# Kernel optimization log

Measured on AMD Instinct MI355X. Metric: run time of the kernel, lower is better.

The kernel has to match this reference:

```python
import jax, jax.numpy as jnp
import numpy as np

B, S, H = 1, 2048, 2048
NH, KVH, D = 32, 8, 64
G = NH // KVH  # num_key_value_groups = 4


def setup_inputs() -> dict:
    key = jax.random.key(0)
    k1, k2, k3 = jax.random.split(key, 3)
    x = jax.random.normal(k1, (B, S, H), dtype=jnp.float32)
    w_qkv = jax.random.normal(k2, ((NH + 2 * KVH) * D, H), dtype=jnp.float32) * 0.02
    w_o = jax.random.normal(k3, (H, NH * D), dtype=jnp.float32) * 0.02
    return {"x": x, "w_qkv": w_qkv, "w_o": w_o}


def _rope_cos_sin(seqlen, dim, dtype):
    inv_freq = 1.0 / (10000.0 ** (jnp.arange(0, dim, 2, dtype=jnp.float32) / dim))
    t = jnp.arange(seqlen, dtype=jnp.float32)
    freqs = jnp.outer(t, inv_freq)  # [S, D/2]
    return jnp.cos(freqs).astype(dtype), jnp.sin(freqs).astype(dtype)


def _apply_rope(x, cos, sin):
    # x: [B,S,h,D]; non-interleaved half rotation (flash-attn RotaryEmbedding)
    d2 = x.shape[-1] // 2
    x1, x2 = x[..., :d2], x[..., d2:]
    c = cos[None, :, None, :]
    s = sin[None, :, None, :]
    return jnp.concatenate([x1 * c - x2 * s, x2 * c + x1 * s], axis=-1)


def reference(x, w_qkv, w_o):
    b, s, _ = x.shape
    qkv = x @ w_qkv.T  # fused QKV proj: [B,S,(NH+2*KVH)*D]
    q, kv = jnp.split(qkv, [NH * D], axis=-1)
    q = q.reshape(b, s, NH, D)
    kv = kv.reshape(b, s, 2, KVH, D)
    cos, sin = _rope_cos_sin(s, D, x.dtype)
    q = _apply_rope(q, cos, sin)
    k = _apply_rope(kv[:, :, 0], cos, sin)
    v = kv[:, :, 1]
    # GQA: group q heads per kv head instead of repeat_interleave (same math)
    qg = q.reshape(b, s, KVH, G, D)
    scale = 1.0 / np.sqrt(D).astype(np.float32)
    scores = jnp.einsum('bskgd,btkd->bkgst', qg, k) * scale  # [B,KVH,G,S,S]
    causal = jnp.tril(jnp.ones((s, s), dtype=bool))
    scores = jnp.where(causal[None, None, None], scores, jnp.asarray(-jnp.inf, scores.dtype))
    p = jax.nn.softmax(scores, axis=-1)
    out = jnp.einsum('bkgst,btkd->bskgd', p, v).reshape(b, s, NH * D)
    return out @ w_o.T
```

## Files before the change

kernel.cpp:

```cpp
#include <hip/hip_runtime.h>


typedef __bf16 bf16_t;
typedef __attribute__((ext_vector_type(8))) __bf16 bf16x8;
typedef __attribute__((ext_vector_type(4))) __bf16 bf16x4;
typedef __attribute__((ext_vector_type(4))) float f32x4;

#define S_LEN 2048
#define H_DIM 2048
#define NHEAD 32
#define KVH 8
#define HD 64
#define QKV_N 3072

#define ENT_STRIDE 8320

__global__ void cast3_kernel(const float* __restrict__ x, const float* __restrict__ wq,
                             const float* __restrict__ wo, bf16_t* __restrict__ xb,
                             bf16_t* __restrict__ wqb, bf16_t* __restrict__ wob) {
  int i = blockIdx.x * blockDim.x + threadIdx.x;
  const int n1 = S_LEN * H_DIM / 4, n2 = QKV_N * H_DIM / 4, n3 = H_DIM * H_DIM / 4;
  const float* src; bf16_t* dst; int j;
  if (i < n1)           { src = x;  dst = xb;  j = i; }
  else if (i < n1 + n2) { src = wq; dst = wqb; j = i - n1; }
  else if (i < n1 + n2 + n3) { src = wo; dst = wob; j = i - n1 - n2; }
  else return;
  float4 v = ((const float4*)src)[j];
  bf16x4 o;
  o.x = (bf16_t)v.x; o.y = (bf16_t)v.y; o.z = (bf16_t)v.z; o.w = (bf16_t)v.w;
  ((bf16x4*)dst)[j] = o;
}

__device__ __forceinline__ void async_copy16(bf16_t* lds_base, const bf16_t* g) {
  __builtin_amdgcn_global_load_lds(
      (const __attribute__((address_space(1))) unsigned int*)g,
      (__attribute__((address_space(3))) unsigned int*)lds_base, 16, 0, 0);
}

#define GBM 128
#define GBN 128

template <int EPI>
__global__ __launch_bounds__(512, 4) void gemm_sk(const bf16_t* __restrict__ A,
                                                  const bf16_t* __restrict__ B,
                                                  float* __restrict__ C,
                                                  bf16_t* __restrict__ qb,
                                                  bf16_t* __restrict__ ktp,
                                                  bf16_t* __restrict__ vt2,
                                                  int M, int N, int K) {
  __shared__ __align__(16) bf16_t As[2][GBM * 64];
  __shared__ __align__(16) bf16_t Bs[2][GBM * 64];

  const int tid  = threadIdx.x;
  const int lane = tid & 63;
  const int w    = tid >> 6;
  const int wq   = w & 3;
  const int gw   = w >> 2;
  const int wm   = (wq >> 1) * 64;
  const int wn   = (wq & 1) * 64;
  const int c    = lane & 15;
  const int quad = lane >> 4;
  const int m0   = blockIdx.y * GBM;
  const int n0   = blockIdx.x * GBN;

  f32x4 acc[4][4] = {};

  const bf16_t* Ab = A + (size_t)m0 * K;
  const bf16_t* Bb = B + (size_t)n0 * K;

  int srow[2], skc[2], sb[2];
#pragma unroll
  for (int i = 0; i < 2; ++i) {
    int p = i * 512 + tid;
    srow[i] = p >> 3;
    skc[i]  = (p & 7) ^ (srow[i] & 7);
    sb[i]   = (i * 512 + w * 64) * 8;
  }

  auto stage = [&](int buf, int k0) {
#pragma unroll
    for (int i = 0; i < 2; ++i) {
      async_copy16(&As[buf][sb[i]], Ab + (size_t)srow[i] * K + k0 + skc[i] * 8);
      async_copy16(&Bs[buf][sb[i]], Bb + (size_t)srow[i] * K + k0 + skc[i] * 8);
    }
  };

  auto compute = [&](int buf) {
    bf16x8 af[4], bfr[4];
#pragma unroll
    for (int mt = 0; mt < 4; ++mt) {
      int row = wm + mt * 16 + c;
      af[mt] = *(const bf16x8*)&As[buf][(row * 8 + ((gw * 4 + quad) ^ (row & 7))) * 8];
    }
#pragma unroll
    for (int nt = 0; nt < 4; ++nt) {
      int rowb = wn + nt * 16 + c;
      bfr[nt] = *(const bf16x8*)&Bs[buf][(rowb * 8 + ((gw * 4 + quad) ^ (rowb & 7))) * 8];
    }
#pragma unroll
    for (int mt = 0; mt < 4; ++mt)
#pragma unroll
      for (int nt = 0; nt < 4; ++nt)
        acc[mt][nt] = __builtin_amdgcn_mfma_f32_16x16x32_bf16(af[mt], bfr[nt], acc[mt][nt], 0, 0, 0);
  };

  const int NI = K >> 6;
  stage(0, 0);
  int buf = 0;
  for (int it = 0; it < NI; ++it) {
    asm volatile("s_waitcnt vmcnt(0)" ::: "memory");
    __builtin_amdgcn_s_barrier();
    if (it + 1 < NI) stage(buf ^ 1, (it + 1) << 6);
    compute(buf);
    buf ^= 1;
  }

  __syncthreads();
  float* xch = (float*)&As[0][0];
  if (gw == 1) {
#pragma unroll
    for (int t16 = 0; t16 < 16; ++t16)
      *(f32x4*)&xch[wq * 4096 + (t16 * 64 + lane) * 4] = acc[t16 >> 2][t16 & 3];
  }
  __syncthreads();
  if (gw == 0) {
#pragma unroll
    for (int t16 = 0; t16 < 16; ++t16) {
      f32x4 o = *(const f32x4*)&xch[wq * 4096 + (t16 * 64 + lane) * 4];
      acc[t16 >> 2][t16 & 3] += o;
    }

    if (EPI == 0) {
#pragma unroll
      for (int mt = 0; mt < 4; ++mt)
#pragma unroll
        for (int nt = 0; nt < 4; ++nt)
#pragma unroll
          for (int reg = 0; reg < 4; ++reg) {
            int row = m0 + wm + mt * 16 + quad * 4 + reg;
            int col = n0 + wn + nt * 16 + c;
            C[(size_t)row * N + col] = acc[mt][nt][reg];
          }
    } else {
      const int colb = n0 + wn;
      if (colb < NHEAD * HD) {
        const int h = colb >> 6;
#pragma unroll
        for (int nt = 0; nt < 2; ++nt) {
          const int i = nt * 16 + c;
          const float invf = __expf(-(float)i * (9.210340371976184f / 32.0f));
#pragma unroll
          for (int mt = 0; mt < 4; ++mt)
#pragma unroll
            for (int reg = 0; reg < 4; ++reg) {
              const int s = m0 + wm + mt * 16 + quad * 4 + reg;
              float sn, cs;
              __sincosf((float)s * invf, &sn, &cs);
              const float x1 = acc[mt][nt][reg], x2 = acc[mt][nt + 2][reg];
              bf16_t* q = qb + (size_t)s * H_DIM + h * HD;
              q[i]      = (bf16_t)((x1 * cs - x2 * sn) * 0.125f);
              q[i + 32] = (bf16_t)((x2 * cs + x1 * sn) * 0.125f);
            }
        }
      } else if (colb < NHEAD * HD + KVH * HD) {
        const int kh = (colb - NHEAD * HD) >> 6;
#pragma unroll
        for (int nt = 0; nt < 2; ++nt) {
          const int i = nt * 16 + c;
          const float invf = __expf(-(float)i * (9.210340371976184f / 32.0f));
#pragma unroll
          for (int mt = 0; mt < 4; ++mt)
#pragma unroll
            for (int reg = 0; reg < 4; ++reg) {
              const int s = m0 + wm + mt * 16 + quad * 4 + reg;
              float sn, cs;
              __sincosf((float)s * invf, &sn, &cs);
              const float x1 = acc[mt][nt][reg], x2 = acc[mt][nt + 2][reg];
              bf16_t* kd = ktp + ((size_t)kh * S_LEN + s) * HD;
              kd[i]      = (bf16_t)(x1 * cs - x2 * sn);
              kd[i + 32] = (bf16_t)(x2 * cs + x1 * sn);
            }
        }
      } else {
        const int kh = (colb - NHEAD * HD - KVH * HD) >> 6;
#pragma unroll
        for (int nt = 0; nt < 4; ++nt) {
          const int d = nt * 16 + c;
#pragma unroll
          for (int mt = 0; mt < 4; ++mt) {
            const int sr = m0 + wm + mt * 16 + quad * 4;
            bf16x4 pv;
#pragma unroll
            for (int reg = 0; reg < 4; ++reg) pv[reg] = (bf16_t)acc[mt][nt][reg];
            *(bf16x4*)&vt2[((size_t)kh * HD + d) * S_LEN + sr] = pv;
          }
        }
      }
    }
  }
}

#define PSTR 72

__global__ __launch_bounds__(256) void flash_split(const bf16_t* __restrict__ qb,
                                                   const bf16_t* __restrict__ kt,
                                                   const bf16_t* __restrict__ vt2,
                                                   float* __restrict__ pbuf,
                                                   bf16_t* __restrict__ attn) {
  __shared__ __align__(16) bf16_t Ks[64 * 64];
  __shared__ __align__(16) bf16_t Vs[64 * 64];
  __shared__ __align__(16) bf16_t Ps[4][32 * PSTR];

  const int tid  = threadIdx.x;
  const int lane = tid & 63;
  const int w    = tid >> 6;
  const int e    = (int)gridDim.x - 1 - (int)blockIdx.x;
  const int kh   = e / 160;
  const int i    = e - kh * 160;

  int qt, t_begin, t_end;
  {
    int T;
    if (i < 16)      { qt = i;                T = (qt >> 1) + 1; t_begin = 0;                 t_end = T; }
    else if (i < 48) { int r = i - 16; qt = 16 + (r >> 1); int ck = r & 1;
                       T = (qt >> 1) + 1; t_begin = (ck * T) >> 1;      t_end = ((ck + 1) * T) >> 1; }
    else if (i < 96) { int r = i - 48; qt = 32 + r / 3;    int ck = r % 3;
                       T = (qt >> 1) + 1; t_begin = (ck * T) / 3;       t_end = ((ck + 1) * T) / 3; }
    else             { int r = i - 96; qt = 48 + (r >> 2); int ck = r & 3;
                       T = (qt >> 1) + 1; t_begin = (ck * T) >> 2;      t_end = ((ck + 1) * T) >> 2; }
  }
  const int T     = (qt >> 1) + 1;
  const int s0    = qt * 32;
  const int h     = kh * 4 + w;
  const int c     = lane & 15;
  const int quad  = lane >> 4;

  bf16x8 qf[2][2];
#pragma unroll
  for (int rf = 0; rf < 2; ++rf)
#pragma unroll
    for (int ks = 0; ks < 2; ++ks)
      qf[rf][ks] = *(const bf16x8*)(qb + (size_t)(s0 + rf * 16 + c) * H_DIM + h * HD + ks * 32 + quad * 8);

  f32x4 acc[2][4] = {};
  float lsum[2] = {0.f, 0.f};

  const bf16_t* kbase = kt + (size_t)kh * S_LEN * HD;
  const bf16_t* vbase = vt2 + (size_t)kh * HD * S_LEN;

  int srow[2], skc[2], sbase[2];
#pragma unroll
  for (int i2 = 0; i2 < 2; ++i2) {
    int chunkbase = i2 * 256 + w * 64;
    int p = chunkbase + lane;
    sbase[i2] = chunkbase * 8;
    srow[i2]  = p >> 3;
    skc[i2]   = (p & 7) ^ (srow[i2] & 7);
  }

  for (int tile = t_begin; tile < t_end; ++tile) {
    const int t0 = tile * 64;
    __syncthreads();
#pragma unroll
    for (int i2 = 0; i2 < 2; ++i2) {
      async_copy16(&Ks[sbase[i2]], kbase + (size_t)(t0 + srow[i2]) * HD + skc[i2] * 8);
      async_copy16(&Vs[sbase[i2]], vbase + (size_t)srow[i2] * S_LEN + t0 + skc[i2] * 8);
    }
    __syncthreads();

    const bool masked = (tile == T - 1);
    int nact = 4;
    if (masked) { nact = ((s0 + 31 - t0) >> 4) + 1; if (nact > 4) nact = 4; }
    const int nkh = (nact + 1) >> 1;

#pragma unroll
    for (int rf = 0; rf < 2; ++rf) {
      for (int kt2 = 0; kt2 < nact; ++kt2) {
        f32x4 st = {};
#pragma unroll
        for (int ks = 0; ks < 2; ++ks) {
          bf16x8 kf = *(const bf16x8*)&Ks[((kt2 * 16 + c) * 8 + ((ks * 4 + quad) ^ (c & 7))) * 8];
          st = __builtin_amdgcn_mfma_f32_16x16x32_bf16(kf, qf[rf][ks], st, 0, 0, 0);
        }
        const int row = s0 + rf * 16 + c;
        bf16x4 pk;
#pragma unroll
        for (int reg = 0; reg < 4; ++reg) {
          const int key = t0 + kt2 * 16 + quad * 4 + reg;
          float p = __expf(st[reg] - 8.0f);
          if (masked && key > row) p = 0.f;
          pk[reg] = (bf16_t)p;
          lsum[rf] += p;
        }
        *(bf16x4*)&Ps[w][(rf * 16 + c) * PSTR + kt2 * 16 + quad * 4] = pk;
      }
      for (int kt2 = nact; kt2 < 2 * nkh; ++kt2) {
        bf16x4 z = {};
        *(bf16x4*)&Ps[w][(rf * 16 + c) * PSTR + kt2 * 16 + quad * 4] = z;
      }
    }

    for (int kh2 = 0; kh2 < nkh; ++kh2) {
      bf16x8 vf[4];
#pragma unroll
      for (int dt = 0; dt < 4; ++dt)
        vf[dt] = *(const bf16x8*)&Vs[((dt * 16 + c) * 8 + ((kh2 * 4 + quad) ^ (c & 7))) * 8];
#pragma unroll
      for (int rf = 0; rf < 2; ++rf) {
        bf16x8 pa = *(const bf16x8*)&Ps[w][(rf * 16 + c) * PSTR + kh2 * 32 + quad * 8];
#pragma unroll
        for (int dt = 0; dt < 4; ++dt)
          acc[rf][dt] = __builtin_amdgcn_mfma_f32_16x16x32_bf16(pa, vf[dt], acc[rf][dt], 0, 0, 0);
      }
    }
  }

#pragma unroll
  for (int rf = 0; rf < 2; ++rf) {
    lsum[rf] += __shfl_xor(lsum[rf], 16);
    lsum[rf] += __shfl_xor(lsum[rf], 32);
  }

  if (i < 16) {
    float* lbuf = (float*)&Ps[w][0];
#pragma unroll
    for (int rf = 0; rf < 2; ++rf) lbuf[rf * 16 + c] = lsum[rf];
    asm volatile("s_waitcnt lgkmcnt(0)" ::: "memory");
#pragma unroll
    for (int rf = 0; rf < 2; ++rf)
#pragma unroll
      for (int reg = 0; reg < 4; ++reg) {
        const float inv = 1.0f / lbuf[rf * 16 + quad * 4 + reg];
        const int row = s0 + rf * 16 + quad * 4 + reg;
#pragma unroll
        for (int dt = 0; dt < 4; ++dt)
          attn[(size_t)row * H_DIM + h * HD + dt * 16 + c] = (bf16_t)(acc[rf][dt][reg] * inv);
      }
  } else {
    float* ent = pbuf + (size_t)e * ENT_STRIDE;
#pragma unroll
    for (int rf = 0; rf < 2; ++rf) {
#pragma unroll
      for (int dt = 0; dt < 4; ++dt)
#pragma unroll
        for (int reg = 0; reg < 4; ++reg)
          ent[w * 2048 + (rf * 16 + quad * 4 + reg) * 64 + dt * 16 + c] = acc[rf][dt][reg];
      ent[8192 + w * 32 + rf * 16 + c] = lsum[rf];
    }
  }
}

__global__ __launch_bounds__(256) void flash_reduce(const float* __restrict__ pbuf,
                                                    bf16_t* __restrict__ attn) {
  const int kh = blockIdx.x / 48;
  const int qt = 16 + (blockIdx.x % 48);
  const int b  = qt >> 4;
  int base;
  if (b == 1)      base = kh * 160 + 16 + (qt - 16) * 2;
  else if (b == 2) base = kh * 160 + 48 + (qt - 32) * 3;
  else             base = kh * 160 + 96 + (qt - 48) * 4;
  const int nch = b + 1;

  const int t   = threadIdx.x;
  const int h2  = t >> 6;
  const int row = (t >> 1) & 31;
  const int dh  = t & 1;

  f32x4 o[8] = {};
  float l = 0.f;
  for (int ci = 0; ci < nch; ++ci) {
    const float* ent = pbuf + (size_t)(base + ci) * ENT_STRIDE;
    const float* p = ent + h2 * 2048 + row * 64 + dh * 32;
#pragma unroll
    for (int j = 0; j < 8; ++j) {
      f32x4 v = ((const f32x4*)p)[j];
      o[j][0] += v[0]; o[j][1] += v[1]; o[j][2] += v[2]; o[j][3] += v[3];
    }
    l += ent[8192 + h2 * 32 + row];
  }
  const float inv = 1.0f / l;
  bf16_t* dst = attn + (size_t)(qt * 32 + row) * H_DIM + (kh * 4 + h2) * 64 + dh * 32;
#pragma unroll
  for (int j = 0; j < 8; ++j) {
    bf16x4 ov;
    ov[0] = (bf16_t)(o[j][0] * inv); ov[1] = (bf16_t)(o[j][1] * inv);
    ov[2] = (bf16_t)(o[j][2] * inv); ov[3] = (bf16_t)(o[j][3] * inv);
    *(bf16x4*)(dst + j * 4) = ov;
  }
}

extern "C" void kernel_launch(void* const* d_in, const int* in_sizes, int n_in,
                              void* d_out, int out_size, void* d_ws, size_t ws_size,
                              hipStream_t stream) {
  const float* x     = (const float*)d_in[0];
  const float* w_qkv = (const float*)d_in[1];
  const float* w_o   = (const float*)d_in[2];
  float* out = (float*)d_out;

  char* ws = (char*)d_ws;
  const size_t OVERLAY = (size_t)1280 * ENT_STRIDE * 4;
  bf16_t* x_bf    = (bf16_t*)ws;
  bf16_t* wqkv_bf = (bf16_t*)(ws + (size_t)S_LEN * H_DIM * 2);
  float*  pbuf    = (float*)ws;
  size_t off = OVERLAY;
  bf16_t* wo_bf   = (bf16_t*)(ws + off); off += (size_t)H_DIM * H_DIM * 2;
  bf16_t* q_bf    = (bf16_t*)(ws + off); off += (size_t)S_LEN * H_DIM * 2;
  bf16_t* k_t     = (bf16_t*)(ws + off); off += (size_t)KVH * S_LEN * HD * 2;
  bf16_t* v_t2    = (bf16_t*)(ws + off); off += (size_t)KVH * S_LEN * HD * 2;
  bf16_t* attn    = (bf16_t*)(ws + off); off += (size_t)S_LEN * H_DIM * 2;

  const int ntot = (S_LEN * H_DIM + QKV_N * H_DIM + H_DIM * H_DIM) / 4;
  cast3_kernel<<<(ntot + 255) / 256, 256, 0, stream>>>(x, w_qkv, w_o, x_bf, wqkv_bf, wo_bf);

  gemm_sk<1><<<dim3(QKV_N / GBN, S_LEN / GBM), 512, 0, stream>>>(
      x_bf, wqkv_bf, nullptr, q_bf, k_t, v_t2, S_LEN, QKV_N, H_DIM);

  flash_split<<<1280, 256, 0, stream>>>(q_bf, k_t, v_t2, pbuf, attn);
  flash_reduce<<<384, 256, 0, stream>>>(pbuf, attn);

  gemm_sk<0><<<dim3(H_DIM / GBN, S_LEN / GBM), 512, 0, stream>>>(
      attn, wo_bf, out, nullptr, nullptr, nullptr, S_LEN, H_DIM, H_DIM);
}
```

Before: 217.6 us.

## Double-buffer K/V tiles through registers and raise MFMA wave priority in flash kernel

Replaces the per-tile async global-to-LDS copies, which sat between two barriers, with a register double buffer. The next K/V tile is loaded into registers while the current one is written to LDS and computed, so global latency can overlap compute. It also hoists the K fragment loads out of the row-fragment loop, wraps the MFMA sequences in s_setprio, restricts the P zero-fill to masked tiles, and adds a waves-per-EU hint to launch_bounds. The costs are extra VGPRs for the buffers and a less reliable barrier that uses raw s_barrier with a manual waitcnt.

```diff
diff --git a/kernel.cpp b/kernel.cpp
--- a/kernel.cpp
+++ b/kernel.cpp
@@ -202,11 +202,11 @@
 
 #define PSTR 72
 
-__global__ __launch_bounds__(256) void flash_split(const bf16_t* __restrict__ qb,
-                                                   const bf16_t* __restrict__ kt,
-                                                   const bf16_t* __restrict__ vt2,
-                                                   float* __restrict__ pbuf,
-                                                   bf16_t* __restrict__ attn) {
+__global__ __launch_bounds__(256, 4) void flash_split(const bf16_t* __restrict__ qb,
+                                                      const bf16_t* __restrict__ kt,
+                                                      const bf16_t* __restrict__ vt2,
+                                                      float* __restrict__ pbuf,
+                                                      bf16_t* __restrict__ attn) {
   __shared__ __align__(16) bf16_t Ks[64 * 64];
   __shared__ __align__(16) bf16_t Vs[64 * 64];
   __shared__ __align__(16) bf16_t Ps[4][32 * PSTR];
@@ -258,30 +258,56 @@
     skc[i2]   = (p & 7) ^ (srow[i2] & 7);
   }
 
+  bf16x8 kA[2], vA[2], kB[2], vB[2];
+  auto ldregs = [&](bf16x8 kr[2], bf16x8 vr[2], int tile) {
+    const int t0 = tile * 64;
+#pragma unroll
+    for (int i2 = 0; i2 < 2; ++i2) {
+      kr[i2] = *(const bf16x8*)(kbase + (size_t)(t0 + srow[i2]) * HD + skc[i2] * 8);
+      vr[i2] = *(const bf16x8*)(vbase + (size_t)srow[i2] * S_LEN + t0 + skc[i2] * 8);
+    }
+  };
+  auto wrlds = [&](bf16x8 kr[2], bf16x8 vr[2]) {
+#pragma unroll
+    for (int i2 = 0; i2 < 2; ++i2) {
+      *(bf16x8*)&Ks[sbase[i2] + lane * 8] = kr[i2];
+      *(bf16x8*)&Vs[sbase[i2] + lane * 8] = vr[i2];
+    }
+  };
+
+  ldregs(kA, vA, t_begin);
+  int phase = 0;
   for (int tile = t_begin; tile < t_end; ++tile) {
     const int t0 = tile * 64;
-    __syncthreads();
-#pragma unroll
-    for (int i2 = 0; i2 < 2; ++i2) {
-      async_copy16(&Ks[sbase[i2]], kbase + (size_t)(t0 + srow[i2]) * HD + skc[i2] * 8);
-      async_copy16(&Vs[sbase[i2]], vbase + (size_t)srow[i2] * S_LEN + t0 + skc[i2] * 8);
-    }
-    __syncthreads();
+    __builtin_amdgcn_s_barrier();
+    if (phase == 0) {
+      wrlds(kA, vA);
+      if (tile + 1 < t_end) ldregs(kB, vB, tile + 1);
+    } else {
+      wrlds(kB, vB);
+      if (tile + 1 < t_end) ldregs(kA, vA, tile + 1);
+    }
+    asm volatile("s_waitcnt lgkmcnt(0)" ::: "memory");
+    __builtin_amdgcn_s_barrier();
+    phase ^= 1;
 
     const bool masked = (tile == T - 1);
     int nact = 4;
     if (masked) { nact = ((s0 + 31 - t0) >> 4) + 1; if (nact > 4) nact = 4; }
     const int nkh = (nact + 1) >> 1;
 
-#pragma unroll
-    for (int rf = 0; rf < 2; ++rf) {
-      for (int kt2 = 0; kt2 < nact; ++kt2) {
+    for (int kt2 = 0; kt2 < nact; ++kt2) {
+      bf16x8 kf[2];
+#pragma unroll
+      for (int ks = 0; ks < 2; ++ks)
+        kf[ks] = *(const bf16x8*)&Ks[((kt2 * 16 + c) * 8 + ((ks * 4 + quad) ^ (c & 7))) * 8];
+#pragma unroll
+      for (int rf = 0; rf < 2; ++rf) {
         f32x4 st = {};
-#pragma unroll
-        for (int ks = 0; ks < 2; ++ks) {
-          bf16x8 kf = *(const bf16x8*)&Ks[((kt2 * 16 + c) * 8 + ((ks * 4 + quad) ^ (c & 7))) * 8];
-          st = __builtin_amdgcn_mfma_f32_16x16x32_bf16(kf, qf[rf][ks], st, 0, 0, 0);
-        }
+        __builtin_amdgcn_s_setprio(1);
+        st = __builtin_amdgcn_mfma_f32_16x16x32_bf16(kf[0], qf[rf][0], st, 0, 0, 0);
+        st = __builtin_amdgcn_mfma_f32_16x16x32_bf16(kf[1], qf[rf][1], st, 0, 0, 0);
+        __builtin_amdgcn_s_setprio(0);
         const int row = s0 + rf * 16 + c;
         bf16x4 pk;
 #pragma unroll
@@ -294,10 +320,14 @@
         }
         *(bf16x4*)&Ps[w][(rf * 16 + c) * PSTR + kt2 * 16 + quad * 4] = pk;
       }
-      for (int kt2 = nact; kt2 < 2 * nkh; ++kt2) {
-        bf16x4 z = {};
-        *(bf16x4*)&Ps[w][(rf * 16 + c) * PSTR + kt2 * 16 + quad * 4] = z;
-      }
+    }
+    if (masked) {
+#pragma unroll
+      for (int rf = 0; rf < 2; ++rf)
+        for (int kt2 = nact; kt2 < 2 * nkh; ++kt2) {
+          bf16x4 z = {};
+          *(bf16x4*)&Ps[w][(rf * 16 + c) * PSTR + kt2 * 16 + quad * 4] = z;
+        }
     }
 
     for (int kh2 = 0; kh2 < nkh; ++kh2) {
@@ -305,6 +335,7 @@
 #pragma unroll
       for (int dt = 0; dt < 4; ++dt)
         vf[dt] = *(const bf16x8*)&Vs[((dt * 16 + c) * 8 + ((kh2 * 4 + quad) ^ (c & 7))) * 8];
+      __builtin_amdgcn_s_setprio(1);
 #pragma unroll
       for (int rf = 0; rf < 2; ++rf) {
         bf16x8 pa = *(const bf16x8*)&Ps[w][(rf * 16 + c) * PSTR + kh2 * 32 + quad * 8];
@@ -312,6 +343,7 @@
         for (int dt = 0; dt < 4; ++dt)
           acc[rf][dt] = __builtin_amdgcn_mfma_f32_16x16x32_bf16(pa, vf[dt], acc[rf][dt], 0, 0, 0);
       }
+      __builtin_amdgcn_s_setprio(0);
     }
   }
 
```

New measurement: 221.2 us. Within noise of the previous version (+1.7%).
